# Optimization experiments

Hardware: AMD Instinct MI355X
Metric: run time of the kernel (lower is better)

Reference implementation:

```python
import jax, jax.numpy as jnp
import numpy as np

D_MODEL = 256
NUM_HEADS = 4
EPS = 1e-6


def setup_inputs() -> dict:
    key = jax.random.key(0)
    ks = jax.random.split(key, 9)
    B, T, D = 4, 2048, D_MODEL
    scale = 1.0 / np.sqrt(D)
    inp = {
        "x": jax.random.normal(ks[0], (B, T, D), dtype=jnp.float32),
        "Wq": jax.random.normal(ks[1], (D, D), dtype=jnp.float32) * scale,
        "bq": jnp.zeros((D,), dtype=jnp.float32),
        "Wk": jax.random.normal(ks[2], (D, D), dtype=jnp.float32) * scale,
        "bk": jnp.zeros((D,), dtype=jnp.float32),
        "Wv": jax.random.normal(ks[3], (D, D), dtype=jnp.float32) * scale,
        "bv": jnp.zeros((D,), dtype=jnp.float32),
        "Wo": jax.random.normal(ks[4], (D, D), dtype=jnp.float32) * scale,
        "bo": jnp.zeros((D,), dtype=jnp.float32),
    }
    return inp


def _feature_map(a):
    # F.elu(x) + 1.0
    return jax.nn.elu(a) + 1.0


def reference(x, Wq, bq, Wk, bk, Wv, bv, Wo, bo):
    B, T, D = x.shape
    H = NUM_HEADS
    dh = D // H
    Q = _feature_map((x @ Wq + bq).reshape(B, T, H, dh))
    K = _feature_map((x @ Wk + bk).reshape(B, T, H, dh))
    V = (x @ Wv + bv).reshape(B, T, H, dh)
    # outer-product state: (B,T,H,dh,dh), cumulative over time
    KV = jnp.einsum('bthd,bthm->bthdm', K, V)
    S = jnp.cumsum(KV, axis=1)
    Z = jnp.cumsum(K, axis=1)
    out = jnp.einsum('bthd,bthdm->bthm', Q, S)
    denom = jnp.einsum('bthd,bthd->bth', Q, Z)[..., None] + EPS
    out = (out / denom).reshape(B, T, D)
    return out @ Wo + bo
```

## Files before the change

### kernel.cpp

```cpp
#include <hip/hip_runtime.h>
#include <hip/hip_bf16.h>

#define D_MODEL 256
#define NHEADS 4
#define DHEAD 64
#define BATCH 4
#define TSEQ 2048
#define CHUNK 64
#define NCHUNK (TSEQ / CHUNK)
#define NTOK (BATCH * TSEQ)
#define NBH (BATCH * NHEADS)
#define EPSV 1e-6f
#define LSTRF 68

typedef __bf16 bf16x8 __attribute__((ext_vector_type(8)));
typedef float f32x4 __attribute__((ext_vector_type(4)));
typedef unsigned short us8 __attribute__((ext_vector_type(8)));

__device__ __forceinline__ float elu1(float a) {
    return a > 0.0f ? a + 1.0f : __expf(a);
}

__device__ __forceinline__ unsigned short f2bf(float f) {
    __hip_bfloat16 h = __float2bfloat16(f);
    return __builtin_bit_cast(unsigned short, h);
}

__device__ __forceinline__ float bf2f(unsigned short u) {
    return __bfloat162float(__builtin_bit_cast(__hip_bfloat16, u));
}

__device__ __forceinline__ bf16x8 frag8(const float* p) {
    const float4 x = *reinterpret_cast<const float4*>(p);
    const float4 y = *reinterpret_cast<const float4*>(p + 4);
    us8 u;
    u[0] = f2bf(x.x); u[1] = f2bf(x.y); u[2] = f2bf(x.z); u[3] = f2bf(x.w);
    u[4] = f2bf(y.x); u[5] = f2bf(y.y); u[6] = f2bf(y.z); u[7] = f2bf(y.w);
    return __builtin_bit_cast(bf16x8, u);
}

__device__ __forceinline__ void gld_lds16(const void* g, void* l) {
    __builtin_amdgcn_global_load_lds(
        (const __attribute__((address_space(1))) void*)g,
        (__attribute__((address_space(3))) void*)l, 16, 0, 0);
}

__global__ __launch_bounds__(256) void convert_x_kernel(
    const float* __restrict__ x, unsigned short* __restrict__ xb)
{
    const int i = (blockIdx.x * 256 + threadIdx.x) * 8;
    const float4 a = *reinterpret_cast<const float4*>(&x[i]);
    const float4 b = *reinterpret_cast<const float4*>(&x[i + 4]);
    ushort4 u0 = { f2bf(a.x), f2bf(a.y), f2bf(a.z), f2bf(a.w) };
    ushort4 u1 = { f2bf(b.x), f2bf(b.y), f2bf(b.z), f2bf(b.w) };
    *reinterpret_cast<ushort4*>(&xb[i]) = u0;
    *reinterpret_cast<ushort4*>(&xb[i + 4]) = u1;
}

__global__ __launch_bounds__(256) void convert_w_kernel(
    const float* __restrict__ Wq, const float* __restrict__ Wk,
    const float* __restrict__ Wv, const float* __restrict__ Wo,
    unsigned short* __restrict__ Wt, unsigned short* __restrict__ Wot)
{
    __shared__ float Ls[64][65];
    const int tid = threadIdx.x;
    const int wi = blockIdx.x >> 4;
    const int ti = blockIdx.x & 15;
    const int k0 = (ti >> 2) * 64, n0 = (ti & 3) * 64;
    const float* W = wi == 0 ? Wq : wi == 1 ? Wk : wi == 2 ? Wv : Wo;
#pragma unroll
    for (int i = 0; i < 16; ++i) {
        const int idx = i * 256 + tid;
        const int r = idx >> 6, c = idx & 63;
        Ls[r][c] = W[(size_t)(k0 + r) * D_MODEL + n0 + c];
    }
    __syncthreads();
    unsigned short* outp = (wi < 3) ? (Wt + (size_t)(wi * 256 + n0) * D_MODEL + k0)
                                    : (Wot + (size_t)n0 * D_MODEL + k0);
#pragma unroll
    for (int i = 0; i < 16; ++i) {
        const int idx = i * 256 + tid;
        const int rn = idx >> 6, ck = idx & 63;
        outp[(size_t)rn * D_MODEL + ck] = f2bf(Ls[ck][rn]);
    }
}

template<int MODE>
__global__ __launch_bounds__(256) void mfma_gemm_kernel(
    const unsigned short* __restrict__ A,
    const unsigned short* __restrict__ Bt,
    const float* __restrict__ b0, const float* __restrict__ b1,
    const float* __restrict__ b2,
    void* __restrict__ O0, void* __restrict__ O1, void* __restrict__ O2)
{
    __shared__ __align__(16) unsigned short As[128 * 64];
    __shared__ __align__(16) unsigned short Bs[128 * 64];
    const int tid = threadIdx.x;
    const int wave = tid >> 6, lane = tid & 63;
    const int la = lane & 15, q = lane >> 4;
    const int wm = (wave >> 1) * 64, wn = (wave & 1) * 64;

    int mtile, ntile;
    if (MODE == 0) { ntile = blockIdx.x % 6; mtile = blockIdx.x / 6; }
    else           { ntile = blockIdx.x & 1; mtile = blockIdx.x >> 1; }
    const int m0 = mtile * 128, n0 = ntile * 128;

    const unsigned short* Ab = A  + (size_t)m0 * D_MODEL;
    const unsigned short* Bb = Bt + (size_t)n0 * D_MODEL;

    f32x4 acc[4][4];
#pragma unroll
    for (int i = 0; i < 4; ++i)
#pragma unroll
        for (int j = 0; j < 4; ++j) acc[i][j] = (f32x4){0.f, 0.f, 0.f, 0.f};

    for (int k0 = 0; k0 < D_MODEL; k0 += 64) {
#pragma unroll
        for (int i = 0; i < 4; ++i) {
            const int bslot = i * 256 + wave * 64;
            const int slot = bslot + lane;
            const int m = slot >> 3, s = slot & 7;
            const int g = s ^ (m & 7);
            gld_lds16(Ab + (size_t)m * D_MODEL + k0 + g * 8, &As[bslot * 8]);
            gld_lds16(Bb + (size_t)m * D_MODEL + k0 + g * 8, &Bs[bslot * 8]);
        }
        __syncthreads();

        bf16x8 af[4][2], bfr[4][2];
#pragma unroll
        for (int i = 0; i < 4; ++i) {
#pragma unroll
            for (int kh = 0; kh < 2; ++kh) {
                const int g = kh * 4 + q;
                const int m = wm + i * 16 + la;
                af[i][kh] = *reinterpret_cast<const bf16x8*>(
                    &As[m * 64 + ((g ^ (m & 7)) << 3)]);
                const int n = wn + i * 16 + la;
                bfr[i][kh] = *reinterpret_cast<const bf16x8*>(
                    &Bs[n * 64 + ((g ^ (n & 7)) << 3)]);
            }
        }
#pragma unroll
        for (int mi = 0; mi < 4; ++mi)
#pragma unroll
            for (int ni = 0; ni < 4; ++ni) {
                acc[mi][ni] = __builtin_amdgcn_mfma_f32_16x16x32_bf16(
                    af[mi][0], bfr[ni][0], acc[mi][ni], 0, 0, 0);
                acc[mi][ni] = __builtin_amdgcn_mfma_f32_16x16x32_bf16(
                    af[mi][1], bfr[ni][1], acc[mi][ni], 0, 0, 0);
            }
        __syncthreads();
    }

#pragma unroll
    for (int mi = 0; mi < 4; ++mi) {
#pragma unroll
        for (int ni = 0; ni < 4; ++ni) {
            const int row = m0 + wm + mi * 16 + q * 4;
            const int col = n0 + wn + ni * 16 + la;
            if (MODE == 0) {
                const int which = col >> 8;
                const int cl = col & 255;
                unsigned short* Out = (unsigned short*)
                    (which == 0 ? O0 : which == 1 ? O1 : O2);
                const float* bias = which == 0 ? b0 : which == 1 ? b1 : b2;
                const int act = (which < 2);
                const float bv = bias[cl];
#pragma unroll
                for (int r = 0; r < 4; ++r) {
                    float v = acc[mi][ni][r] + bv;
                    if (act) v = elu1(v);
                    Out[(size_t)(row + r) * D_MODEL + cl] = f2bf(v);
                }
            } else {
                float* Out = (float*)O0;
                const float bv = b0[col];
#pragma unroll
                for (int r = 0; r < 4; ++r)
                    Out[(size_t)(row + r) * D_MODEL + col] = acc[mi][ni][r] + bv;
            }
        }
    }
}

__global__ __launch_bounds__(256) void chunksum_kernel(
    const unsigned short* __restrict__ Kb, const unsigned short* __restrict__ Vb,
    float* __restrict__ Pt, float* __restrict__ Zc)
{
    __shared__ float Ktf[DHEAD * LSTRF];
    __shared__ float Vtf[DHEAD * LSTRF];
    const int tid = threadIdx.x;
    const int c  = blockIdx.x % NCHUNK;
    const int bh = blockIdx.x / NCHUNK;
    const int b = bh / NHEADS, h = bh % NHEADS;
    const size_t gbase = ((size_t)(b * TSEQ + c * CHUNK)) * D_MODEL + h * DHEAD;

#pragma unroll
    for (int i = 0; i < 16; ++i) {
        const int idx = i * 256 + tid;
        const int t = idx >> 6, d = idx & 63;
        Ktf[d * LSTRF + t] = bf2f(Kb[gbase + (size_t)t * D_MODEL + d]);
        Vtf[d * LSTRF + t] = bf2f(Vb[gbase + (size_t)t * D_MODEL + d]);
    }
    __syncthreads();

    const int wave = tid >> 6, lane = tid & 63;
    const int la = lane & 15, q = lane >> 4;
    const int wm = (wave >> 1) * 32, wn = (wave & 1) * 32;

    f32x4 acc[2][2];
#pragma unroll
    for (int i = 0; i < 2; ++i)
#pragma unroll
        for (int j = 0; j < 2; ++j) acc[i][j] = (f32x4){0.f, 0.f, 0.f, 0.f};

#pragma unroll
    for (int ks = 0; ks < 2; ++ks) {
        const int ko = ks * 32 + q * 8;
        const bf16x8 a0  = frag8(&Vtf[(wm + la) * LSTRF + ko]);
        const bf16x8 a1  = frag8(&Vtf[(wm + 16 + la) * LSTRF + ko]);
        const bf16x8 bb0 = frag8(&Ktf[(wn + la) * LSTRF + ko]);
        const bf16x8 bb1 = frag8(&Ktf[(wn + 16 + la) * LSTRF + ko]);
        acc[0][0] = __builtin_amdgcn_mfma_f32_16x16x32_bf16(a0, bb0, acc[0][0], 0, 0, 0);
        acc[0][1] = __builtin_amdgcn_mfma_f32_16x16x32_bf16(a0, bb1, acc[0][1], 0, 0, 0);
        acc[1][0] = __builtin_amdgcn_mfma_f32_16x16x32_bf16(a1, bb0, acc[1][0], 0, 0, 0);
        acc[1][1] = __builtin_amdgcn_mfma_f32_16x16x32_bf16(a1, bb1, acc[1][1], 0, 0, 0);
    }

    float* Pb = Pt + (size_t)blockIdx.x * (DHEAD * DHEAD);
#pragma unroll
    for (int mi = 0; mi < 2; ++mi)
#pragma unroll
        for (int ni = 0; ni < 2; ++ni) {
            const int row = wm + mi * 16 + q * 4;
            const int col = wn + ni * 16 + la;
#pragma unroll
            for (int r = 0; r < 4; ++r)
                Pb[(row + r) * DHEAD + col] = acc[mi][ni][r];
        }

    if (tid < DHEAD) {
        float z = 0.f;
        for (int t = 0; t < CHUNK; ++t) z += Ktf[tid * LSTRF + t];
        Zc[(size_t)blockIdx.x * DHEAD + tid] = z;
    }
}

__global__ __launch_bounds__(256) void prefix_kernel(
    float* __restrict__ P, float* __restrict__ Zc)
{
    const int tid = threadIdx.x;
    if (blockIdx.x < NBH * 16) {
        const int bh = blockIdx.x >> 4;
        const int e = ((blockIdx.x & 15) << 8) + tid;
        const size_t base = (size_t)bh * NCHUNK * (DHEAD * DHEAD) + e;
        float v[NCHUNK];
#pragma unroll
        for (int c = 0; c < NCHUNK; ++c) v[c] = P[base + (size_t)c * (DHEAD * DHEAD)];
        float s = 0.f;
#pragma unroll
        for (int c = 0; c < NCHUNK; ++c) {
            const float t = v[c];
            P[base + (size_t)c * (DHEAD * DHEAD)] = s;
            s += t;
        }
    } else {
        const int j = ((int)(blockIdx.x - NBH * 16) << 8) + tid;
        if (j < NBH * DHEAD) {
            const int bh = j >> 6, d = j & 63;
            float v[NCHUNK];
#pragma unroll
            for (int c = 0; c < NCHUNK; ++c) v[c] = Zc[(bh * NCHUNK + c) * DHEAD + d];
            float s = 0.f;
#pragma unroll
            for (int c = 0; c < NCHUNK; ++c) {
                const float t = v[c];
                Zc[(bh * NCHUNK + c) * DHEAD + d] = s;
                s += t;
            }
        }
    }
}

__global__ __launch_bounds__(256) void chunkout_kernel(
    const unsigned short* __restrict__ Qb, const unsigned short* __restrict__ Kb,
    const unsigned short* __restrict__ Vb,
    const float* __restrict__ Pt, const float* __restrict__ Zx,
    unsigned short* __restrict__ Ob)
{
    __shared__ float Qs[CHUNK * LSTRF];
    __shared__ float Ks[CHUNK * LSTRF];
    __shared__ float Vtf[DHEAD * LSTRF];
    __shared__ float At[CHUNK * LSTRF];
    __shared__ float zsh[DHEAD];
    __shared__ float dnm[CHUNK];

    const int tid = threadIdx.x;
    const int c  = blockIdx.x % NCHUNK;
    const int bh = blockIdx.x / NCHUNK;
    const int b = bh / NHEADS, h = bh % NHEADS;
    const size_t gbase = ((size_t)(b * TSEQ + c * CHUNK)) * D_MODEL + h * DHEAD;
    const float* Pp = Pt + (size_t)blockIdx.x * (DHEAD * DHEAD);

#pragma unroll
    for (int i = 0; i < 16; ++i) {
        const int idx = i * 256 + tid;
        const int t = idx >> 6, d = idx & 63;
        const float qv = bf2f(Qb[gbase + (size_t)t * D_MODEL + d]);
        const float kv = bf2f(Kb[gbase + (size_t)t * D_MODEL + d]);
        const float vv = bf2f(Vb[gbase + (size_t)t * D_MODEL + d]);
        Qs[t * LSTRF + d]  = qv;
        Ks[t * LSTRF + d]  = kv;
        Vtf[d * LSTRF + t] = vv;
    }
    if (tid < DHEAD) zsh[tid] = Zx[((size_t)bh * NCHUNK + c) * DHEAD + tid];
    __syncthreads();

    const int wave = tid >> 6, lane = tid & 63;
    const int la = lane & 15, q = lane >> 4;
    const int wt = (wave >> 1) * 32, wn = (wave & 1) * 32;

    f32x4 acc[2][2];
#pragma unroll
    for (int i = 0; i < 2; ++i)
#pragma unroll
        for (int j = 0; j < 2; ++j) acc[i][j] = (f32x4){0.f, 0.f, 0.f, 0.f};
#pragma unroll
    for (int ks = 0; ks < 2; ++ks) {
        const int ko = ks * 32 + q * 8;
        const bf16x8 a0  = frag8(&Qs[(wt + la) * LSTRF + ko]);
        const bf16x8 a1  = frag8(&Qs[(wt + 16 + la) * LSTRF + ko]);
        const bf16x8 bb0 = frag8(&Ks[(wn + la) * LSTRF + ko]);
        const bf16x8 bb1 = frag8(&Ks[(wn + 16 + la) * LSTRF + ko]);
        acc[0][0] = __builtin_amdgcn_mfma_f32_16x16x32_bf16(a0, bb0, acc[0][0], 0, 0, 0);
        acc[0][1] = __builtin_amdgcn_mfma_f32_16x16x32_bf16(a0, bb1, acc[0][1], 0, 0, 0);
        acc[1][0] = __builtin_amdgcn_mfma_f32_16x16x32_bf16(a1, bb0, acc[1][0], 0, 0, 0);
        acc[1][1] = __builtin_amdgcn_mfma_f32_16x16x32_bf16(a1, bb1, acc[1][1], 0, 0, 0);
    }
#pragma unroll
    for (int mi = 0; mi < 2; ++mi)
#pragma unroll
        for (int ni = 0; ni < 2; ++ni) {
            const int t0 = wt + mi * 16 + q * 4;
            const int s  = wn + ni * 16 + la;
#pragma unroll
            for (int r = 0; r < 4; ++r)
                At[(t0 + r) * LSTRF + s] = (s <= t0 + r) ? acc[mi][ni][r] : 0.f;
        }
    __syncthreads();

    if (tid < CHUNK) {
        float dv = 0.f;
        for (int s = 0; s < CHUNK; ++s) dv += At[tid * LSTRF + s];
        for (int d = 0; d < DHEAD; ++d) dv = fmaf(Qs[tid * LSTRF + d], zsh[d], dv);
        dnm[tid] = dv + EPSV;
    }
    __syncthreads();

    f32x4 o[2][2];
#pragma unroll
    for (int i = 0; i < 2; ++i)
#pragma unroll
        for (int j = 0; j < 2; ++j) o[i][j] = (f32x4){0.f, 0.f, 0.f, 0.f};
#pragma unroll
    for (int ks = 0; ks < 2; ++ks) {
        const int ko = ks * 32 + q * 8;
        const bf16x8 a0  = frag8(&Qs[(wt + la) * LSTRF + ko]);
        const bf16x8 a1  = frag8(&Qs[(wt + 16 + la) * LSTRF + ko]);
        const bf16x8 bb0 = frag8(&Pp[(wn + la) * DHEAD + ko]);
        const bf16x8 bb1 = frag8(&Pp[(wn + 16 + la) * DHEAD + ko]);
        o[0][0] = __builtin_amdgcn_mfma_f32_16x16x32_bf16(a0, bb0, o[0][0], 0, 0, 0);
        o[0][1] = __builtin_amdgcn_mfma_f32_16x16x32_bf16(a0, bb1, o[0][1], 0, 0, 0);
        o[1][0] = __builtin_amdgcn_mfma_f32_16x16x32_bf16(a1, bb0, o[1][0], 0, 0, 0);
        o[1][1] = __builtin_amdgcn_mfma_f32_16x16x32_bf16(a1, bb1, o[1][1], 0, 0, 0);
    }
#pragma unroll
    for (int ks = 0; ks < 2; ++ks) {
        const int ko = ks * 32 + q * 8;
        const bf16x8 a0  = frag8(&At[(wt + la) * LSTRF + ko]);
        const bf16x8 a1  = frag8(&At[(wt + 16 + la) * LSTRF + ko]);
        const bf16x8 bb0 = frag8(&Vtf[(wn + la) * LSTRF + ko]);
        const bf16x8 bb1 = frag8(&Vtf[(wn + 16 + la) * LSTRF + ko]);
        o[0][0] = __builtin_amdgcn_mfma_f32_16x16x32_bf16(a0, bb0, o[0][0], 0, 0, 0);
        o[0][1] = __builtin_amdgcn_mfma_f32_16x16x32_bf16(a0, bb1, o[0][1], 0, 0, 0);
        o[1][0] = __builtin_amdgcn_mfma_f32_16x16x32_bf16(a1, bb0, o[1][0], 0, 0, 0);
        o[1][1] = __builtin_amdgcn_mfma_f32_16x16x32_bf16(a1, bb1, o[1][1], 0, 0, 0);
    }

#pragma unroll
    for (int mi = 0; mi < 2; ++mi)
#pragma unroll
        for (int ni = 0; ni < 2; ++ni) {
            const int t0 = wt + mi * 16 + q * 4;
            const int m  = wn + ni * 16 + la;
#pragma unroll
            for (int r = 0; r < 4; ++r) {
                const float v = o[mi][ni][r] / dnm[t0 + r];
                Ob[gbase + (size_t)(t0 + r) * D_MODEL + m] = f2bf(v);
            }
        }
}

extern "C" void kernel_launch(void* const* d_in, const int* in_sizes, int n_in,
                              void* d_out, int out_size, void* d_ws, size_t ws_size,
                              hipStream_t stream)
{
    const float* x  = (const float*)d_in[0];
    const float* Wq = (const float*)d_in[1];
    const float* bq = (const float*)d_in[2];
    const float* Wk = (const float*)d_in[3];
    const float* bk = (const float*)d_in[4];
    const float* Wv = (const float*)d_in[5];
    const float* bv = (const float*)d_in[6];
    const float* Wo = (const float*)d_in[7];
    const float* bo = (const float*)d_in[8];
    float* out = (float*)d_out;

    const size_t NE = (size_t)NTOK * D_MODEL;
    unsigned short* xb  = (unsigned short*)d_ws;
    unsigned short* Wt  = xb + NE;
    unsigned short* Wot = Wt + 768 * 256;
    unsigned short* Qb  = Wot + 256 * 256;
    unsigned short* Kb  = Qb + NE;
    unsigned short* Vb  = Kb + NE;
    unsigned short* Ob  = Vb + NE;
    float* P = (float*)(Ob + NE);
    float* Z = P + (size_t)NBH * NCHUNK * DHEAD * DHEAD;

    convert_x_kernel<<<NTOK * D_MODEL / 8 / 256, 256, 0, stream>>>(x, xb);
    convert_w_kernel<<<64, 256, 0, stream>>>(Wq, Wk, Wv, Wo, Wt, Wot);
    mfma_gemm_kernel<0><<<(NTOK / 128) * 6, 256, 0, stream>>>(
        xb, Wt, bq, bk, bv, Qb, Kb, Vb);
    chunksum_kernel<<<NBH * NCHUNK, 256, 0, stream>>>(Kb, Vb, P, Z);
    prefix_kernel<<<NBH * 16 + 4, 256, 0, stream>>>(P, Z);
    chunkout_kernel<<<NBH * NCHUNK, 256, 0, stream>>>(Qb, Kb, Vb, P, Z, Ob);
    mfma_gemm_kernel<1><<<(NTOK / 128) * 2, 256, 0, stream>>>(
        Ob, Wot, bo, nullptr, nullptr, out, nullptr, nullptr);
}
```

Before: 117.0 us.

## Fuse convert kernels, drop prefix kernel, vectorize bf16 tile loads

```diff
diff --git a/kernel.cpp b/kernel.cpp
--- a/kernel.cpp
+++ b/kernel.cpp
@@ -12,6 +12,7 @@
 #define NBH (BATCH * NHEADS)
 #define EPSV 1e-6f
 #define LSTRF 68
+#define PSTR 36
 
 typedef __bf16 bf16x8 __attribute__((ext_vector_type(8)));
 typedef float f32x4 __attribute__((ext_vector_type(4)));
@@ -28,6 +29,22 @@
 
 __device__ __forceinline__ float bf2f(unsigned short u) {
     return __bfloat162float(__builtin_bit_cast(__hip_bfloat16, u));
+}
+
+__device__ __forceinline__ void unpack2(unsigned int u, float& lo, float& hi) {
+    lo = __builtin_bit_cast(float, u << 16);
+    hi = __builtin_bit_cast(float, u & 0xFFFF0000u);
+}
+
+__device__ __forceinline__ void unpack8(uint4 u, float* f) {
+    unpack2(u.x, f[0], f[1]);
+    unpack2(u.y, f[2], f[3]);
+    unpack2(u.z, f[4], f[5]);
+    unpack2(u.w, f[6], f[7]);
+}
+
+__device__ __forceinline__ unsigned int pack2(float a, float b) {
+    return (unsigned int)f2bf(a) | ((unsigned int)f2bf(b) << 16);
 }
 
 __device__ __forceinline__ bf16x8 frag8(const float* p) {
@@ -45,27 +62,28 @@
         (__attribute__((address_space(3))) void*)l, 16, 0, 0);
 }
 
-__global__ __launch_bounds__(256) void convert_x_kernel(
-    const float* __restrict__ x, unsigned short* __restrict__ xb)
-{
-    const int i = (blockIdx.x * 256 + threadIdx.x) * 8;
-    const float4 a = *reinterpret_cast<const float4*>(&x[i]);
-    const float4 b = *reinterpret_cast<const float4*>(&x[i + 4]);
-    ushort4 u0 = { f2bf(a.x), f2bf(a.y), f2bf(a.z), f2bf(a.w) };
-    ushort4 u1 = { f2bf(b.x), f2bf(b.y), f2bf(b.z), f2bf(b.w) };
-    *reinterpret_cast<ushort4*>(&xb[i]) = u0;
-    *reinterpret_cast<ushort4*>(&xb[i + 4]) = u1;
-}
-
-__global__ __launch_bounds__(256) void convert_w_kernel(
+__global__ __launch_bounds__(256) void convert_kernel(
+    const float* __restrict__ x,
     const float* __restrict__ Wq, const float* __restrict__ Wk,
     const float* __restrict__ Wv, const float* __restrict__ Wo,
+    unsigned short* __restrict__ xb,
     unsigned short* __restrict__ Wt, unsigned short* __restrict__ Wot)
 {
+    const int tid = threadIdx.x;
+    if (blockIdx.x < NTOK * D_MODEL / 8 / 256) {
+        const int i = (blockIdx.x * 256 + tid) * 8;
+        const float4 a = *reinterpret_cast<const float4*>(&x[i]);
+        const float4 b = *reinterpret_cast<const float4*>(&x[i + 4]);
+        ushort4 u0 = { f2bf(a.x), f2bf(a.y), f2bf(a.z), f2bf(a.w) };
+        ushort4 u1 = { f2bf(b.x), f2bf(b.y), f2bf(b.z), f2bf(b.w) };
+        *reinterpret_cast<ushort4*>(&xb[i]) = u0;
+        *reinterpret_cast<ushort4*>(&xb[i + 4]) = u1;
+        return;
+    }
     __shared__ float Ls[64][65];
-    const int tid = threadIdx.x;
-    const int wi = blockIdx.x >> 4;
-    const int ti = blockIdx.x & 15;
+    const int bid = blockIdx.x - NTOK * D_MODEL / 8 / 256;
+    const int wi = bid >> 4;
+    const int ti = bid & 15;
     const int k0 = (ti >> 2) * 64, n0 = (ti & 3) * 64;
     const float* W = wi == 0 ? Wq : wi == 1 ? Wk : wi == 2 ? Wv : Wo;
 #pragma unroll
@@ -187,8 +205,8 @@
     const unsigned short* __restrict__ Kb, const unsigned short* __restrict__ Vb,
     float* __restrict__ Pt, float* __restrict__ Zc)
 {
-    __shared__ float Ktf[DHEAD * LSTRF];
-    __shared__ float Vtf[DHEAD * LSTRF];
+    __shared__ __align__(16) float Ktf[DHEAD * LSTRF];
+    __shared__ __align__(16) float Vtf[DHEAD * LSTRF];
     const int tid = threadIdx.x;
     const int c  = blockIdx.x % NCHUNK;
     const int bh = blockIdx.x / NCHUNK;
@@ -196,11 +214,17 @@
     const size_t gbase = ((size_t)(b * TSEQ + c * CHUNK)) * D_MODEL + h * DHEAD;
 
 #pragma unroll
-    for (int i = 0; i < 16; ++i) {
+    for (int i = 0; i < 2; ++i) {
         const int idx = i * 256 + tid;
-        const int t = idx >> 6, d = idx & 63;
-        Ktf[d * LSTRF + t] = bf2f(Kb[gbase + (size_t)t * D_MODEL + d]);
-        Vtf[d * LSTRF + t] = bf2f(Vb[gbase + (size_t)t * D_MODEL + d]);
+        const int t = idx >> 3, e0 = (idx & 7) * 8;
+        float kf[8], vf[8];
+        unpack8(*reinterpret_cast<const uint4*>(&Kb[gbase + (size_t)t * D_MODEL + e0]), kf);
+        unpack8(*reinterpret_cast<const uint4*>(&Vb[gbase + (size_t)t * D_MODEL + e0]), vf);
+#pragma unroll
+        for (int j = 0; j < 8; ++j) {
+            Ktf[(e0 + j) * LSTRF + t] = kf[j];
+            Vtf[(e0 + j) * LSTRF + t] = vf[j];
+        }
     }
     __syncthreads();
 
@@ -246,52 +270,17 @@
     }
 }
 
-__global__ __launch_bounds__(256) void prefix_kernel(
-    float* __restrict__ P, float* __restrict__ Zc)
-{
-    const int tid = threadIdx.x;
-    if (blockIdx.x < NBH * 16) {
-        const int bh = blockIdx.x >> 4;
-        const int e = ((blockIdx.x & 15) << 8) + tid;
-        const size_t base = (size_t)bh * NCHUNK * (DHEAD * DHEAD) + e;
-        float v[NCHUNK];
-#pragma unroll
-        for (int c = 0; c < NCHUNK; ++c) v[c] = P[base + (size_t)c * (DHEAD * DHEAD)];
-        float s = 0.f;
-#pragma unroll
-        for (int c = 0; c < NCHUNK; ++c) {
-            const float t = v[c];
-            P[base + (size_t)c * (DHEAD * DHEAD)] = s;
-            s += t;
-        }
-    } else {
-        const int j = ((int)(blockIdx.x - NBH * 16) << 8) + tid;
-        if (j < NBH * DHEAD) {
-            const int bh = j >> 6, d = j & 63;
-            float v[NCHUNK];
-#pragma unroll
-            for (int c = 0; c < NCHUNK; ++c) v[c] = Zc[(bh * NCHUNK + c) * DHEAD + d];
-            float s = 0.f;
-#pragma unroll
-            for (int c = 0; c < NCHUNK; ++c) {
-                const float t = v[c];
-                Zc[(bh * NCHUNK + c) * DHEAD + d] = s;
-                s += t;
-            }
-        }
-    }
-}
-
 __global__ __launch_bounds__(256) void chunkout_kernel(
     const unsigned short* __restrict__ Qb, const unsigned short* __restrict__ Kb,
     const unsigned short* __restrict__ Vb,
-    const float* __restrict__ Pt, const float* __restrict__ Zx,
+    const float* __restrict__ Pt, const float* __restrict__ Zc,
     unsigned short* __restrict__ Ob)
 {
-    __shared__ float Qs[CHUNK * LSTRF];
-    __shared__ float Ks[CHUNK * LSTRF];
-    __shared__ float Vtf[DHEAD * LSTRF];
-    __shared__ float At[CHUNK * LSTRF];
+    __shared__ __align__(16) float Qs[CHUNK * LSTRF];
+    __shared__ __align__(16) float Ks[CHUNK * LSTRF];
+    __shared__ __align__(16) float Vtf[DHEAD * LSTRF];
+    __shared__ __align__(16) float At[CHUNK * LSTRF];
+    __shared__ __align__(16) unsigned int Stp[DHEAD * PSTR];
     __shared__ float zsh[DHEAD];
     __shared__ float dnm[CHUNK];
 
@@ -300,20 +289,56 @@
     const int bh = blockIdx.x / NCHUNK;
     const int b = bh / NHEADS, h = bh % NHEADS;
     const size_t gbase = ((size_t)(b * TSEQ + c * CHUNK)) * D_MODEL + h * DHEAD;
-    const float* Pp = Pt + (size_t)blockIdx.x * (DHEAD * DHEAD);
-
-#pragma unroll
-    for (int i = 0; i < 16; ++i) {
+
+#pragma unroll
+    for (int i = 0; i < 2; ++i) {
         const int idx = i * 256 + tid;
-        const int t = idx >> 6, d = idx & 63;
-        const float qv = bf2f(Qb[gbase + (size_t)t * D_MODEL + d]);
-        const float kv = bf2f(Kb[gbase + (size_t)t * D_MODEL + d]);
-        const float vv = bf2f(Vb[gbase + (size_t)t * D_MODEL + d]);
-        Qs[t * LSTRF + d]  = qv;
-        Ks[t * LSTRF + d]  = kv;
-        Vtf[d * LSTRF + t] = vv;
-    }
-    if (tid < DHEAD) zsh[tid] = Zx[((size_t)bh * NCHUNK + c) * DHEAD + tid];
+        const int t = idx >> 3, e0 = (idx & 7) * 8;
+        float qf[8], kf[8], vf[8];
+        unpack8(*reinterpret_cast<const uint4*>(&Qb[gbase + (size_t)t * D_MODEL + e0]), qf);
+        unpack8(*reinterpret_cast<const uint4*>(&Kb[gbase + (size_t)t * D_MODEL + e0]), kf);
+        unpack8(*reinterpret_cast<const uint4*>(&Vb[gbase + (size_t)t * D_MODEL + e0]), vf);
+        *reinterpret_cast<float4*>(&Qs[t * LSTRF + e0])     = (float4){qf[0], qf[1], qf[2], qf[3]};
+        *reinterpret_cast<float4*>(&Qs[t * LSTRF + e0 + 4]) = (float4){qf[4], qf[5], qf[6], qf[7]};
+        *reinterpret_cast<float4*>(&Ks[t * LSTRF + e0])     = (float4){kf[0], kf[1], kf[2], kf[3]};
+        *reinterpret_cast<float4*>(&Ks[t * LSTRF + e0 + 4]) = (float4){kf[4], kf[5], kf[6], kf[7]};
+#pragma unroll
+        for (int j = 0; j < 8; ++j)
+            Vtf[(e0 + j) * LSTRF + t] = vf[j];
+    }
+
+    {
+        const int r = tid >> 2, q16 = tid & 3;
+        float sacc[16];
+#pragma unroll
+        for (int k = 0; k < 16; ++k) sacc[k] = 0.f;
+        const float* Pb = Pt + (size_t)bh * NCHUNK * (DHEAD * DHEAD)
+                             + r * DHEAD + q16 * 16;
+        for (int cp = 0; cp < c; ++cp) {
+            const float* src = Pb + (size_t)cp * (DHEAD * DHEAD);
+#pragma unroll
+            for (int k = 0; k < 4; ++k) {
+                const float4 v = *reinterpret_cast<const float4*>(&src[k * 4]);
+                sacc[k * 4 + 0] += v.x;
+                sacc[k * 4 + 1] += v.y;
+                sacc[k * 4 + 2] += v.z;
+                sacc[k * 4 + 3] += v.w;
+            }
+        }
+        uint4 pa, pb2;
+        pa.x  = pack2(sacc[0],  sacc[1]);  pa.y  = pack2(sacc[2],  sacc[3]);
+        pa.z  = pack2(sacc[4],  sacc[5]);  pa.w  = pack2(sacc[6],  sacc[7]);
+        pb2.x = pack2(sacc[8],  sacc[9]);  pb2.y = pack2(sacc[10], sacc[11]);
+        pb2.z = pack2(sacc[12], sacc[13]); pb2.w = pack2(sacc[14], sacc[15]);
+        *reinterpret_cast<uint4*>(&Stp[r * PSTR + q16 * 8])     = pa;
+        *reinterpret_cast<uint4*>(&Stp[r * PSTR + q16 * 8 + 4]) = pb2;
+    }
+    if (tid < DHEAD) {
+        float z = 0.f;
+        for (int cp = 0; cp < c; ++cp)
+            z += Zc[((size_t)bh * NCHUNK + cp) * DHEAD + tid];
+        zsh[tid] = z;
+    }
     __syncthreads();
 
     const int wave = tid >> 6, lane = tid & 63;
@@ -367,8 +392,10 @@
         const int ko = ks * 32 + q * 8;
         const bf16x8 a0  = frag8(&Qs[(wt + la) * LSTRF + ko]);
         const bf16x8 a1  = frag8(&Qs[(wt + 16 + la) * LSTRF + ko]);
-        const bf16x8 bb0 = frag8(&Pp[(wn + la) * DHEAD + ko]);
-        const bf16x8 bb1 = frag8(&Pp[(wn + 16 + la) * DHEAD + ko]);
+        const bf16x8 bb0 = __builtin_bit_cast(bf16x8,
+            *reinterpret_cast<const uint4*>(&Stp[(wn + la) * PSTR + ks * 16 + q * 4]));
+        const bf16x8 bb1 = __builtin_bit_cast(bf16x8,
+            *reinterpret_cast<const uint4*>(&Stp[(wn + 16 + la) * PSTR + ks * 16 + q * 4]));
         o[0][0] = __builtin_amdgcn_mfma_f32_16x16x32_bf16(a0, bb0, o[0][0], 0, 0, 0);
         o[0][1] = __builtin_amdgcn_mfma_f32_16x16x32_bf16(a0, bb1, o[0][1], 0, 0, 0);
         o[1][0] = __builtin_amdgcn_mfma_f32_16x16x32_bf16(a1, bb0, o[1][0], 0, 0, 0);
@@ -427,12 +454,11 @@
     float* P = (float*)(Ob + NE);
     float* Z = P + (size_t)NBH * NCHUNK * DHEAD * DHEAD;
 
-    convert_x_kernel<<<NTOK * D_MODEL / 8 / 256, 256, 0, stream>>>(x, xb);
-    convert_w_kernel<<<64, 256, 0, stream>>>(Wq, Wk, Wv, Wo, Wt, Wot);
+    convert_kernel<<<NTOK * D_MODEL / 8 / 256 + 64, 256, 0, stream>>>(
+        x, Wq, Wk, Wv, Wo, xb, Wt, Wot);
     mfma_gemm_kernel<0><<<(NTOK / 128) * 6, 256, 0, stream>>>(
         xb, Wt, bq, bk, bv, Qb, Kb, Vb);
     chunksum_kernel<<<NBH * NCHUNK, 256, 0, stream>>>(Kb, Vb, P, Z);
-    prefix_kernel<<<NBH * 16 + 4, 256, 0, stream>>>(P, Z);
     chunkout_kernel<<<NBH * NCHUNK, 256, 0, stream>>>(Qb, Kb, Vb, P, Z, Ob);
     mfma_gemm_kernel<1><<<(NTOK / 128) * 2, 256, 0, stream>>>(
         Ob, Wot, bo, nullptr, nullptr, out, nullptr, nullptr);
```

New measurement: 124.4 us. 1.06x slower.
